# Kernel optimization log

Hardware: AMD Instinct MI355X
Metric: run time of the kernel (lower is better)

The kernel has to match this reference:

```python
import jax, jax.numpy as jnp
import numpy as np

N_EMBD = 768
N_HEAD = 12
B, T = 4, 2048
EPS = 1e-5


def layernorm(x, w, b):
    mu = jnp.mean(x, axis=-1, keepdims=True)
    var = jnp.mean(jnp.square(x - mu), axis=-1, keepdims=True)
    return (x - mu) * jax.lax.rsqrt(var + EPS) * w + b


def setup_inputs() -> dict:
    key = jax.random.key(0)
    ks = jax.random.split(key, 6)
    C = N_EMBD
    s = 0.02
    return {
        "x": jax.random.normal(ks[0], (B, T, C), jnp.float32),
        "ln1_w": jnp.ones((C,), jnp.float32),
        "ln1_b": jnp.zeros((C,), jnp.float32),
        "W_qkv": jax.random.normal(ks[1], (C, 3 * C), jnp.float32) * s,
        "b_qkv": jnp.zeros((3 * C,), jnp.float32),
        "W_attnproj": jax.random.normal(ks[2], (C, C), jnp.float32) * s,
        "b_attnproj": jnp.zeros((C,), jnp.float32),
        "ln2_w": jnp.ones((C,), jnp.float32),
        "ln2_b": jnp.zeros((C,), jnp.float32),
        "W_fc": jax.random.normal(ks[3], (C, 4 * C), jnp.float32) * s,
        "b_fc": jnp.zeros((4 * C,), jnp.float32),
        "W_mlpproj": jax.random.normal(ks[4], (4 * C, C), jnp.float32) * s,
        "b_mlpproj": jnp.zeros((C,), jnp.float32),
    }


def reference(x, ln1_w, ln1_b, W_qkv, b_qkv, W_attnproj, b_attnproj,
              ln2_w, ln2_b, W_fc, b_fc, W_mlpproj, b_mlpproj):
    Bx, Tx, C = x.shape
    H = N_HEAD
    Dh = C // H

    # --- attention branch ---
    h = layernorm(x, ln1_w, ln1_b)
    qkv = h @ W_qkv + b_qkv                       # [B, T, 3C]
    q, k, v = jnp.split(qkv, 3, axis=-1)
    q = q.reshape(Bx, Tx, H, Dh).transpose(0, 2, 1, 3)  # [B, H, T, Dh]
    k = k.reshape(Bx, Tx, H, Dh).transpose(0, 2, 1, 3)
    v = v.reshape(Bx, Tx, H, Dh).transpose(0, 2, 1, 3)
    att = jnp.einsum('bhqd,bhkd->bhqk', q, k) * (1.0 / np.sqrt(Dh))
    att = jax.nn.softmax(att, axis=-1)            # full softmax attention (no mask)
    y = jnp.einsum('bhqk,bhkd->bhqd', att, v)     # [B, H, T, Dh]
    y = y.transpose(0, 2, 1, 3).reshape(Bx, Tx, C)
    y = y @ W_attnproj + b_attnproj
    x = x + y

    # --- MLP branch ---
    h = layernorm(x, ln2_w, ln2_b)
    h = jax.nn.gelu(h @ W_fc + b_fc, approximate=False)
    h = h @ W_mlpproj + b_mlpproj
    return x + h
```

## Files before the change

### kernel.cpp

```cpp
#include <hip/hip_runtime.h>

typedef __bf16 bf16x8 __attribute__((ext_vector_type(8)));
typedef __bf16 bf16x4 __attribute__((ext_vector_type(4)));
typedef float f32x4 __attribute__((ext_vector_type(4)));
typedef unsigned short u16;
typedef unsigned long long u64;

#define GL2LDS(gp, lp) __builtin_amdgcn_global_load_lds(                      \
    (const __attribute__((address_space(1))) void*)(gp),                      \
    (__attribute__((address_space(3))) void*)(lp), 16, 0, 0)

__device__ __forceinline__ u16 f2u(float f) {
    __bf16 h = (__bf16)f;
    return __builtin_bit_cast(u16, h);
}

__device__ __forceinline__ float fexp2(float x) {
    float r;
    asm("v_exp_f32 %0, %1" : "=v"(r) : "v"(x));
    return r;
}

__device__ __forceinline__ float frcp(float x) {
    float r;
    asm("v_rcp_f32 %0, %1" : "=v"(r) : "v"(x));
    return r;
}

__device__ __forceinline__ float gelu(float x) {
    const float a = x * x;
    const float b = fmaf(a, 0.10294323f, 2.30220795f);
    const float u = fexp2(x * b);
    const float r = frcp(1.0f + u);
    return (x > 8.0f) ? x : x * u * r;
}

template <int N>
__device__ __forceinline__ void waitv() {
    if constexpr (N == 0) asm volatile("s_waitcnt vmcnt(0)" ::: "memory");
    else if constexpr (N == 4) asm volatile("s_waitcnt vmcnt(4)" ::: "memory");
    else if constexpr (N == 5) asm volatile("s_waitcnt vmcnt(5)" ::: "memory");
    else if constexpr (N == 6) asm volatile("s_waitcnt vmcnt(6)" ::: "memory");
}

__device__ __forceinline__ f32x4 mfma16(bf16x8 a, bf16x8 b, f32x4 c) {
    return __builtin_amdgcn_mfma_f32_16x16x32_bf16(a, b, c, 0, 0, 0);
}

__global__ __launch_bounds__(256) void transpose_kernel(
    const float* __restrict__ W, u16* __restrict__ Wt, int K, int N) {
    __shared__ float tile[32][33];
    const int tx = threadIdx.x & 31, ty = threadIdx.x >> 5;
    const int n0 = blockIdx.x * 32, k0 = blockIdx.y * 32;
#pragma unroll
    for (int i = 0; i < 4; i++)
        tile[ty + 8 * i][tx] = W[(size_t)(k0 + ty + 8 * i) * N + n0 + tx];
    __syncthreads();
#pragma unroll
    for (int i = 0; i < 4; i++)
        Wt[(size_t)(n0 + ty + 8 * i) * K + k0 + tx] = f2u(tile[tx][ty + 8 * i]);
}

__global__ __launch_bounds__(256) void ln_kernel(
    const float* __restrict__ xin, const float* __restrict__ wgt,
    const float* __restrict__ bia, u16* __restrict__ outp) {
    const int row = blockIdx.x, t = threadIdx.x;
    const float* xr = xin + (size_t)row * 768;
    float v0 = xr[t], v1 = xr[t + 256], v2 = xr[t + 512];
    float s = v0 + v1 + v2;
    float ss = v0 * v0 + v1 * v1 + v2 * v2;
#pragma unroll
    for (int off = 32; off; off >>= 1) {
        s += __shfl_xor(s, off);
        ss += __shfl_xor(ss, off);
    }
    __shared__ float red[8];
    const int w = t >> 6;
    if ((t & 63) == 0) { red[w] = s; red[4 + w] = ss; }
    __syncthreads();
    s  = red[0] + red[1] + red[2] + red[3];
    ss = red[4] + red[5] + red[6] + red[7];
    const float mu = s * (1.f / 768.f);
    const float var = ss * (1.f / 768.f) - mu * mu;
    const float rs = rsqrtf(var + 1e-5f);
    u16* orow = outp + (size_t)row * 768;
    orow[t]       = f2u((v0 - mu) * rs * wgt[t]       + bia[t]);
    orow[t + 256] = f2u((v1 - mu) * rs * wgt[t + 256] + bia[t + 256]);
    orow[t + 512] = f2u((v2 - mu) * rs * wgt[t + 512] + bia[t + 512]);
}

template <int EPI>
__global__ __launch_bounds__(256, 3) void gemm96(
    const u16* __restrict__ A, const u16* __restrict__ Bt,
    const float* __restrict__ bias, void* __restrict__ outp,
    u16* __restrict__ vt, int M, int N, int K) {
    __shared__ __align__(16) u16 As[2][4096];
    __shared__ __align__(16) u16 Bs[2][6144];
    const int t = threadIdx.x;
    const int lane = t & 63, w = t >> 6;
    const int wg0 = blockIdx.y * gridDim.x + blockIdx.x;
    const int xcd = wg0 & 7, loc = wg0 >> 3;
    const int gx = gridDim.x, gy = gridDim.y;
    const int m0 = (xcd * (gy >> 3) + loc / gx) * 128;
    const int n0 = (loc % gx) * 192;
    const int wm = (w >> 1) * 64, wn = (w & 1) * 96;
    const int lq = lane & 15, g = lane >> 4;

    f32x4 acc[4][6];
#pragma unroll
    for (int i = 0; i < 4; i++)
#pragma unroll
        for (int j = 0; j < 6; j++) acc[i][j] = (f32x4){0.f, 0.f, 0.f, 0.f};

    const int srow = t >> 2;
    const int scol = ((t & 3) ^ ((t >> 3) & 3)) * 8;
    const u16* gA0 = A + (size_t)(m0 + srow) * K + scol;
    const u16* gA1 = A + (size_t)(m0 + 64 + srow) * K + scol;
    const u16* gB0 = Bt + (size_t)(n0 + srow) * K + scol;
    const u16* gB1 = Bt + (size_t)(n0 + 64 + srow) * K + scol;
    const u16* gB2 = Bt + (size_t)(n0 + 128 + srow) * K + scol;

    const int cph = (g ^ ((lq >> 1) & 3)) << 4;
    const int KT = K >> 5;

#define STAGE96(buf, kt)                                                      \
    do {                                                                      \
        const int ko_ = (kt) << 5;                                            \
        GL2LDS(gA0 + ko_, (char*)As[buf] + w * 1024);                         \
        GL2LDS(gA1 + ko_, (char*)As[buf] + 4096 + w * 1024);                  \
        GL2LDS(gB0 + ko_, (char*)Bs[buf] + w * 1024);                         \
        GL2LDS(gB1 + ko_, (char*)Bs[buf] + 4096 + w * 1024);                  \
        GL2LDS(gB2 + ko_, (char*)Bs[buf] + 8192 + w * 1024);                  \
    } while (0)

    STAGE96(0, 0);
    STAGE96(1, 1);
    for (int kt = 0; kt < KT; ++kt) {
        if (kt + 1 < KT) waitv<5>(); else waitv<0>();
        __builtin_amdgcn_s_barrier();
        __builtin_amdgcn_sched_barrier(0);
        const char* rA = (char*)As[kt & 1] + (wm + lq) * 64 + cph;
        const char* rB = (char*)Bs[kt & 1] + (wn + lq) * 64 + cph;
        bf16x8 af[4];
#pragma unroll
        for (int m = 0; m < 4; m++) af[m] = *(const bf16x8*)(rA + m * 1024);
        __builtin_amdgcn_s_setprio(1);
#pragma unroll
        for (int n = 0; n < 6; n++) {
            const bf16x8 bfr = *(const bf16x8*)(rB + n * 1024);
#pragma unroll
            for (int m = 0; m < 4; m++)
                acc[m][n] = mfma16(af[m], bfr, acc[m][n]);
        }
        __builtin_amdgcn_s_setprio(0);
        __builtin_amdgcn_sched_barrier(0);
        __builtin_amdgcn_s_barrier();
        if (kt + 2 < KT) STAGE96(kt & 1, kt + 2);
    }
#undef STAGE96

#pragma unroll
    for (int n = 0; n < 6; n++) {
        const int col = n0 + wn + 16 * n + lq;
        const float bv = bias[col];
#pragma unroll
        for (int m = 0; m < 4; m++) {
            const int rbase = m0 + wm + 16 * m + 4 * g;
            if constexpr (EPI == 0) {
                if (col < 1536) {
                    const float qs = (col < 768) ? 0.18033688f : 1.0f;
#pragma unroll
                    for (int r = 0; r < 4; r++) {
                        const size_t idx = (size_t)(rbase + r) * N + col;
                        ((u16*)outp)[idx] = f2u((acc[m][n][r] + bv) * qs);
                    }
                } else {
                    const int d = col - 1536;
                    bf16x4 pk;
#pragma unroll
                    for (int r = 0; r < 4; r++)
                        pk[r] = (__bf16)(acc[m][n][r] + bv);
                    u16* vrow = vt +
                        ((size_t)((rbase >> 11) * 12 + (d >> 6)) * 64 + (d & 63)) * 2048 +
                        (rbase & 2047);
                    *(u64*)vrow = __builtin_bit_cast(u64, pk);
                }
            } else {
#pragma unroll
                for (int r = 0; r < 4; r++) {
                    const size_t idx = (size_t)(rbase + r) * N + col;
                    ((u16*)outp)[idx] = f2u(gelu(acc[m][n][r] + bv));
                }
            }
        }
    }
}

__global__ __launch_bounds__(256, 3) void gemm_k64(
    const u16* __restrict__ A, const u16* __restrict__ Bt,
    const float* __restrict__ bias, const float* __restrict__ res,
    float* __restrict__ outp, int M, int N, int K) {
    __shared__ __align__(16) u16 As[2][4096];
    __shared__ __align__(16) u16 Bs[2][8192];
    const int t = threadIdx.x;
    const int lane = t & 63, w = t >> 6;
    const int wg0 = blockIdx.y * gridDim.x + blockIdx.x;
    const int xcd = wg0 & 7, loc = wg0 >> 3;
    const int gx = gridDim.x, gy = gridDim.y;
    const int m0 = (xcd * (gy >> 3) + loc / gx) * 64;
    const int n0 = (loc % gx) * 128;
    const int wm = (w >> 1) * 32, wn = (w & 1) * 64;
    const int lq = lane & 15, g = lane >> 4;

    f32x4 acc[2][4];
#pragma unroll
    for (int i = 0; i < 2; i++)
#pragma unroll
        for (int j = 0; j < 4; j++) acc[i][j] = (f32x4){0.f, 0.f, 0.f, 0.f};

    const int srow8 = w * 8 + (lane >> 3);
    const int scol = ((lane & 7) ^ (lane >> 3)) * 8;
    const u16* gA_0 = A + (size_t)(m0 + srow8) * K + scol;
    const u16* gA_1 = A + (size_t)(m0 + 32 + srow8) * K + scol;
    const u16* gB_0 = Bt + (size_t)(n0 + srow8) * K + scol;
    const u16* gB_1 = Bt + (size_t)(n0 + 32 + srow8) * K + scol;
    const u16* gB_2 = Bt + (size_t)(n0 + 64 + srow8) * K + scol;
    const u16* gB_3 = Bt + (size_t)(n0 + 96 + srow8) * K + scol;

    const int KT = K >> 6;

#define STAGE64(buf, kt)                                                      \
    do {                                                                      \
        const int ko_ = (kt) << 6;                                            \
        GL2LDS(gA_0 + ko_, (char*)As[buf] + w * 1024);                        \
        GL2LDS(gA_1 + ko_, (char*)As[buf] + 4096 + w * 1024);                 \
        GL2LDS(gB_0 + ko_, (char*)Bs[buf] + w * 1024);                        \
        GL2LDS(gB_1 + ko_, (char*)Bs[buf] + 4096 + w * 1024);                 \
        GL2LDS(gB_2 + ko_, (char*)Bs[buf] + 8192 + w * 1024);                 \
        GL2LDS(gB_3 + ko_, (char*)Bs[buf] + 12288 + w * 1024);                \
    } while (0)

    STAGE64(0, 0);
    STAGE64(1, 1);
    for (int kt = 0; kt < KT; ++kt) {
        if (kt + 1 < KT) waitv<6>(); else waitv<0>();
        __builtin_amdgcn_s_barrier();
        __builtin_amdgcn_sched_barrier(0);
        const char* aB = (char*)As[kt & 1] + (wm + lq) * 128;
        const char* bB = (char*)Bs[kt & 1] + (wn + lq) * 128;
        const int sw = lq & 7;
#pragma unroll
        for (int s = 0; s < 2; s++) {
            const int co = (((s << 2) + g) ^ sw) << 4;
            bf16x8 af[2], bfr[4];
#pragma unroll
            for (int m = 0; m < 2; m++)
                af[m] = *(const bf16x8*)(aB + m * 2048 + co);
#pragma unroll
            for (int n = 0; n < 4; n++)
                bfr[n] = *(const bf16x8*)(bB + n * 2048 + co);
            __builtin_amdgcn_s_setprio(1);
#pragma unroll
            for (int m = 0; m < 2; m++)
#pragma unroll
                for (int n = 0; n < 4; n++)
                    acc[m][n] = mfma16(af[m], bfr[n], acc[m][n]);
            __builtin_amdgcn_s_setprio(0);
        }
        __builtin_amdgcn_sched_barrier(0);
        __builtin_amdgcn_s_barrier();
        if (kt + 2 < KT) STAGE64(kt & 1, kt + 2);
    }
#undef STAGE64

#pragma unroll
    for (int n = 0; n < 4; n++) {
        const int col = n0 + wn + 16 * n + lq;
        const float bv = bias[col];
#pragma unroll
        for (int m = 0; m < 2; m++) {
            const int rbase = m0 + wm + 16 * m + 4 * g;
#pragma unroll
            for (int r = 0; r < 4; r++) {
                const size_t idx = (size_t)(rbase + r) * N + col;
                outp[idx] = acc[m][n][r] + bv + res[idx];
            }
        }
    }
}

__global__ __launch_bounds__(256, 3) void attn_kernel(
    const u16* __restrict__ qkv, const u16* __restrict__ Vt,
    u16* __restrict__ y) {
    __shared__ __align__(16) u16 Ks[8192];
    __shared__ __align__(16) u16 Vts[8192];
    __shared__ __align__(16) u16 Ps[4][2048];
    const int t = threadIdx.x, lane = t & 63, w = t >> 6;
    int wg = blockIdx.y * gridDim.x + blockIdx.x;
    wg = (wg & 7) * ((gridDim.x * gridDim.y) >> 3) + (wg >> 3);
    const int bh = wg / gridDim.x;
    const int b = bh / 12, h = bh % 12;
    const int q0 = (wg % gridDim.x) * 128 + w * 32;
    const int lq = lane & 15, g = lane >> 4;
    const int swz = (lq & 7) << 4;

    bf16x8 qf[2][2];
#pragma unroll
    for (int qh = 0; qh < 2; qh++) {
        const u16* qp =
            qkv + (size_t)(b * 2048 + q0 + qh * 16 + lq) * 2304 + h * 64 + g * 8;
        qf[qh][0] = *(const bf16x8*)(qp);
        qf[qh][1] = *(const bf16x8*)(qp + 32);
    }
    bf16x8 ones;
#pragma unroll
    for (int i = 0; i < 8; i++) ones[i] = (__bf16)1.0f;

    f32x4 acc_o[2][4], acc_s[2];
#pragma unroll
    for (int qh = 0; qh < 2; qh++) {
        acc_s[qh] = (f32x4){0.f, 0.f, 0.f, 0.f};
#pragma unroll
        for (int f = 0; f < 4; f++) acc_o[qh][f] = (f32x4){0.f, 0.f, 0.f, 0.f};
    }

    const int srow = t >> 3, sc = (t & 7) ^ (srow & 7);
    const u16* kg = qkv + 768 + h * 64 + sc * 8 + (size_t)(b * 2048 + srow) * 2304;
    const int vrow = t >> 4, vc = (t & 15) ^ (vrow & 7);
    const u16* vg = Vt + (size_t)(bh * 64 + vrow) * 2048 + vc * 8;

    for (int kt = 0; kt < 16; ++kt) {
        const int k0 = kt * 128;
#pragma unroll
        for (int i = 0; i < 4; i++)
            GL2LDS(kg + (size_t)(k0 + 32 * i) * 2304,
                   (char*)Ks + i * 4096 + w * 1024);
#pragma unroll
        for (int j = 0; j < 4; j++)
            GL2LDS(vg + k0 + j * 32768, (char*)Vts + j * 4096 + w * 1024);
        waitv<0>();
        __builtin_amdgcn_s_barrier();
        __builtin_amdgcn_sched_barrier(0);

#pragma unroll
        for (int half = 0; half < 2; half++) {
            const char* KB = (const char*)Ks + half * 64 * 128;
            f32x4 st[2][4];
            __builtin_amdgcn_s_setprio(1);
#pragma unroll
            for (int kb = 0; kb < 4; kb++) {
                st[0][kb] = (f32x4){0.f, 0.f, 0.f, 0.f};
                st[1][kb] = (f32x4){0.f, 0.f, 0.f, 0.f};
                const char* kr = KB + (kb * 16 + lq) * 128;
#pragma unroll
                for (int dh = 0; dh < 2; dh++) {
                    const bf16x8 kf =
                        *(const bf16x8*)(kr + ((((dh << 2) + g) << 4) ^ swz));
                    st[0][kb] = mfma16(kf, qf[0][dh], st[0][kb]);
                    st[1][kb] = mfma16(kf, qf[1][dh], st[1][kb]);
                }
            }
            __builtin_amdgcn_s_setprio(0);

#pragma unroll
            for (int qh = 0; qh < 2; qh++) {
                char* pw = (char*)Ps[w] + (qh * 16 + lq) * 128 + ((g & 1) << 3);
#pragma unroll
                for (int kb = 0; kb < 4; kb++) {
                    bf16x4 pb;
#pragma unroll
                    for (int r = 0; r < 4; r++)
                        pb[r] = (__bf16)fexp2(st[qh][kb][r]);
                    *(u64*)(pw + ((((kb << 1) + (g >> 1)) << 4) ^ swz)) =
                        __builtin_bit_cast(u64, pb);
                }
            }

            __builtin_amdgcn_s_setprio(1);
#pragma unroll
            for (int kk = 0; kk < 2; kk++) {
                bf16x8 vf[4];
#pragma unroll
                for (int f = 0; f < 4; f++)
                    vf[f] = *(const bf16x8*)(
                        (const char*)Vts + (16 * f + lq) * 256 +
                        ((((half << 3) + (kk << 2) + g) ^ (lq & 7)) << 4));
                const int co = ((kk << 2) + g) << 4;
#pragma unroll
                for (int qh = 0; qh < 2; qh++) {
                    const bf16x8 pf = *(const bf16x8*)(
                        (const char*)Ps[w] + (qh * 16 + lq) * 128 + (co ^ swz));
#pragma unroll
                    for (int f = 0; f < 4; f++)
                        acc_o[qh][f] = mfma16(vf[f], pf, acc_o[qh][f]);
                    acc_s[qh] = mfma16(ones, pf, acc_s[qh]);
                }
            }
            __builtin_amdgcn_s_setprio(0);
        }
        __builtin_amdgcn_sched_barrier(0);
        __builtin_amdgcn_s_barrier();
    }

#pragma unroll
    for (int qh = 0; qh < 2; qh++) {
        const float rinv = frcp(acc_s[qh][0]);
        char* yb = (char*)(y + (size_t)(b * 2048 + q0 + qh * 16 + lq) * 768 +
                           h * 64);
#pragma unroll
        for (int f = 0; f < 4; f++) {
            bf16x4 pk;
#pragma unroll
            for (int r = 0; r < 4; r++) pk[r] = (__bf16)(acc_o[qh][f][r] * rinv);
            *(u64*)(yb + f * 32 + g * 8) = __builtin_bit_cast(u64, pk);
        }
    }
}

extern "C" void kernel_launch(void* const* d_in, const int* in_sizes, int n_in,
                              void* d_out, int out_size, void* d_ws,
                              size_t ws_size, hipStream_t stream) {
    const float* x    = (const float*)d_in[0];
    const float* ln1w = (const float*)d_in[1];
    const float* ln1b = (const float*)d_in[2];
    const float* Wqkv = (const float*)d_in[3];
    const float* bqkv = (const float*)d_in[4];
    const float* Wap  = (const float*)d_in[5];
    const float* bap  = (const float*)d_in[6];
    const float* ln2w = (const float*)d_in[7];
    const float* ln2b = (const float*)d_in[8];
    const float* Wfc  = (const float*)d_in[9];
    const float* bfc  = (const float*)d_in[10];
    const float* Wmp  = (const float*)d_in[11];
    const float* bmp  = (const float*)d_in[12];
    float* out = (float*)d_out;

    char* ws = (char*)d_ws;
    u16* Wt_qkv = (u16*)(ws);
    u16* Wt_ap  = (u16*)(ws + 3538944);
    u16* Wt_fc  = (u16*)(ws + 4718592);
    u16* Wt_mp  = (u16*)(ws + 9437184);
    u16* bufA   = (u16*)(ws + 14155776);
    u16* bufB   = (u16*)(ws + 26738688);
    u16* VtBuf  = (u16*)(ws + 64487424);

    transpose_kernel<<<dim3(72, 24), 256, 0, stream>>>(Wqkv, Wt_qkv, 768, 2304);
    transpose_kernel<<<dim3(24, 24), 256, 0, stream>>>(Wap, Wt_ap, 768, 768);
    transpose_kernel<<<dim3(96, 24), 256, 0, stream>>>(Wfc, Wt_fc, 768, 3072);
    transpose_kernel<<<dim3(24, 96), 256, 0, stream>>>(Wmp, Wt_mp, 3072, 768);

    ln_kernel<<<8192, 256, 0, stream>>>(x, ln1w, ln1b, bufA);
    gemm96<0><<<dim3(12, 64), 256, 0, stream>>>(
        bufA, Wt_qkv, bqkv, bufB, VtBuf, 8192, 2304, 768);
    attn_kernel<<<dim3(16, 48), 256, 0, stream>>>(bufB, VtBuf, bufA);
    gemm_k64<<<dim3(6, 128), 256, 0, stream>>>(
        bufA, Wt_ap, bap, x, out, 8192, 768, 768);
    ln_kernel<<<8192, 256, 0, stream>>>(out, ln2w, ln2b, bufA);
    gemm96<2><<<dim3(16, 64), 256, 0, stream>>>(
        bufA, Wt_fc, bfc, bufB, nullptr, 8192, 3072, 768);
    gemm_k64<<<dim3(6, 128), 256, 0, stream>>>(
        bufB, Wt_mp, bmp, out, out, 8192, 768, 3072);
}
```

Before: 262.7 us.

## Split KV range across warp pairs in attention, each warp covering 64 queries

Each warp now handles 64 query rows instead of 32, and the four warps split the key/value sequence into two halves, so warps 0/1 and 2/3 share query blocks but process different KV ranges. Per iteration, each half's K/V tile is 64 keys instead of one 128-key tile, so every K and V fragment read from LDS feeds twice as many queries. Partial outputs and denominators from warps 2/3 are reduced through shared memory at the end. This costs more accumulator registers (acc_o doubles), which may hurt occupancy at launch bounds (256,3), and adds an LDS reduction step.

```diff
diff --git a/kernel.cpp b/kernel.cpp
--- a/kernel.cpp
+++ b/kernel.cpp
@@ -292,21 +292,22 @@
 __global__ __launch_bounds__(256, 3) void attn_kernel(
     const u16* __restrict__ qkv, const u16* __restrict__ Vt,
     u16* __restrict__ y) {
-    __shared__ __align__(16) u16 Ks[8192];
-    __shared__ __align__(16) u16 Vts[8192];
+    __shared__ __align__(16) u16 Ks[2][4096];
+    __shared__ __align__(16) u16 Vts[2][4096];
     __shared__ __align__(16) u16 Ps[4][2048];
     const int t = threadIdx.x, lane = t & 63, w = t >> 6;
     int wg = blockIdx.y * gridDim.x + blockIdx.x;
     wg = (wg & 7) * ((gridDim.x * gridDim.y) >> 3) + (wg >> 3);
     const int bh = wg / gridDim.x;
     const int b = bh / 12, h = bh % 12;
-    const int q0 = (wg % gridDim.x) * 128 + w * 32;
+    const int q0 = (wg % gridDim.x) * 128 + (w & 1) * 64;
+    const int khalf = w >> 1;
     const int lq = lane & 15, g = lane >> 4;
     const int swz = (lq & 7) << 4;
 
-    bf16x8 qf[2][2];
-#pragma unroll
-    for (int qh = 0; qh < 2; qh++) {
+    bf16x8 qf[4][2];
+#pragma unroll
+    for (int qh = 0; qh < 4; qh++) {
         const u16* qp =
             qkv + (size_t)(b * 2048 + q0 + qh * 16 + lq) * 2304 + h * 64 + g * 8;
         qf[qh][0] = *(const bf16x8*)(qp);
@@ -316,9 +317,9 @@
 #pragma unroll
     for (int i = 0; i < 8; i++) ones[i] = (__bf16)1.0f;
 
-    f32x4 acc_o[2][4], acc_s[2];
-#pragma unroll
-    for (int qh = 0; qh < 2; qh++) {
+    f32x4 acc_o[4][4], acc_s[4];
+#pragma unroll
+    for (int qh = 0; qh < 4; qh++) {
         acc_s[qh] = (f32x4){0.f, 0.f, 0.f, 0.f};
 #pragma unroll
         for (int f = 0; f < 4; f++) acc_o[qh][f] = (f32x4){0.f, 0.f, 0.f, 0.f};
@@ -326,25 +327,29 @@
 
     const int srow = t >> 3, sc = (t & 7) ^ (srow & 7);
     const u16* kg = qkv + 768 + h * 64 + sc * 8 + (size_t)(b * 2048 + srow) * 2304;
-    const int vrow = t >> 4, vc = (t & 15) ^ (vrow & 7);
-    const u16* vg = Vt + (size_t)(bh * 64 + vrow) * 2048 + vc * 8;
+    const u16* vg = Vt + (size_t)(bh * 64 + srow) * 2048 + sc * 8;
+
+    const char* KB = (const char*)Ks + khalf * 8192;
+    const char* VB = (const char*)Vts + khalf * 8192;
 
     for (int kt = 0; kt < 16; ++kt) {
-        const int k0 = kt * 128;
-#pragma unroll
-        for (int i = 0; i < 4; i++)
-            GL2LDS(kg + (size_t)(k0 + 32 * i) * 2304,
-                   (char*)Ks + i * 4096 + w * 1024);
-#pragma unroll
-        for (int j = 0; j < 4; j++)
-            GL2LDS(vg + k0 + j * 32768, (char*)Vts + j * 4096 + w * 1024);
+#pragma unroll
+        for (int hh = 0; hh < 2; hh++) {
+            const int kb0 = hh * 1024 + kt * 64;
+            GL2LDS(kg + (size_t)kb0 * 2304,
+                   (char*)Ks + hh * 8192 + w * 1024);
+            GL2LDS(kg + (size_t)(kb0 + 32) * 2304,
+                   (char*)Ks + hh * 8192 + 4096 + w * 1024);
+            GL2LDS(vg + kb0, (char*)Vts + hh * 8192 + w * 1024);
+            GL2LDS(vg + kb0 + 32 * 2048,
+                   (char*)Vts + hh * 8192 + 4096 + w * 1024);
+        }
         waitv<0>();
         __builtin_amdgcn_s_barrier();
         __builtin_amdgcn_sched_barrier(0);
 
 #pragma unroll
-        for (int half = 0; half < 2; half++) {
-            const char* KB = (const char*)Ks + half * 64 * 128;
+        for (int p = 0; p < 2; p++) {
             f32x4 st[2][4];
             __builtin_amdgcn_s_setprio(1);
 #pragma unroll
@@ -356,21 +361,21 @@
                 for (int dh = 0; dh < 2; dh++) {
                     const bf16x8 kf =
                         *(const bf16x8*)(kr + ((((dh << 2) + g) << 4) ^ swz));
-                    st[0][kb] = mfma16(kf, qf[0][dh], st[0][kb]);
-                    st[1][kb] = mfma16(kf, qf[1][dh], st[1][kb]);
+                    st[0][kb] = mfma16(kf, qf[2 * p][dh], st[0][kb]);
+                    st[1][kb] = mfma16(kf, qf[2 * p + 1][dh], st[1][kb]);
                 }
             }
             __builtin_amdgcn_s_setprio(0);
 
 #pragma unroll
-            for (int qh = 0; qh < 2; qh++) {
-                char* pw = (char*)Ps[w] + (qh * 16 + lq) * 128 + ((g & 1) << 3);
+            for (int e = 0; e < 2; e++) {
+                char* pw = (char*)Ps[w] + (e * 16 + lq) * 128 + ((g & 1) << 3);
 #pragma unroll
                 for (int kb = 0; kb < 4; kb++) {
                     bf16x4 pb;
 #pragma unroll
                     for (int r = 0; r < 4; r++)
-                        pb[r] = (__bf16)fexp2(st[qh][kb][r]);
+                        pb[r] = (__bf16)fexp2(st[e][kb][r]);
                     *(u64*)(pw + ((((kb << 1) + (g >> 1)) << 4) ^ swz)) =
                         __builtin_bit_cast(u64, pb);
                 }
@@ -379,21 +384,21 @@
             __builtin_amdgcn_s_setprio(1);
 #pragma unroll
             for (int kk = 0; kk < 2; kk++) {
+                const int co = ((kk << 2) + g) << 4;
                 bf16x8 vf[4];
 #pragma unroll
                 for (int f = 0; f < 4; f++)
-                    vf[f] = *(const bf16x8*)(
-                        (const char*)Vts + (16 * f + lq) * 256 +
-                        ((((half << 3) + (kk << 2) + g) ^ (lq & 7)) << 4));
-                const int co = ((kk << 2) + g) << 4;
-#pragma unroll
-                for (int qh = 0; qh < 2; qh++) {
+                    vf[f] = *(const bf16x8*)(VB + (16 * f + lq) * 128 +
+                                             (co ^ swz));
+#pragma unroll
+                for (int e = 0; e < 2; e++) {
                     const bf16x8 pf = *(const bf16x8*)(
-                        (const char*)Ps[w] + (qh * 16 + lq) * 128 + (co ^ swz));
+                        (const char*)Ps[w] + (e * 16 + lq) * 128 + (co ^ swz));
 #pragma unroll
                     for (int f = 0; f < 4; f++)
-                        acc_o[qh][f] = mfma16(vf[f], pf, acc_o[qh][f]);
-                    acc_s[qh] = mfma16(ones, pf, acc_s[qh]);
+                        acc_o[2 * p + e][f] =
+                            mfma16(vf[f], pf, acc_o[2 * p + e][f]);
+                    acc_s[2 * p + e] = mfma16(ones, pf, acc_s[2 * p + e]);
                 }
             }
             __builtin_amdgcn_s_setprio(0);
@@ -402,17 +407,38 @@
         __builtin_amdgcn_s_barrier();
     }
 
-#pragma unroll
-    for (int qh = 0; qh < 2; qh++) {
-        const float rinv = frcp(acc_s[qh][0]);
-        char* yb = (char*)(y + (size_t)(b * 2048 + q0 + qh * 16 + lq) * 768 +
-                           h * 64);
-#pragma unroll
-        for (int f = 0; f < 4; f++) {
-            bf16x4 pk;
-#pragma unroll
-            for (int r = 0; r < 4; r++) pk[r] = (__bf16)(acc_o[qh][f][r] * rinv);
-            *(u64*)(yb + f * 32 + g * 8) = __builtin_bit_cast(u64, pk);
+    if (w >= 2) {
+        char* base = (w == 2) ? (char*)Ks : (char*)Vts;
+#pragma unroll
+        for (int qh = 0; qh < 4; qh++)
+#pragma unroll
+            for (int f = 0; f < 4; f++)
+                *(f32x4*)(base + (((qh << 2) + f) * 64 + lane) * 16) =
+                    acc_o[qh][f];
+        float* db = (float*)Ps[0] + (w - 2) * 256;
+#pragma unroll
+        for (int qh = 0; qh < 4; qh++) db[qh * 64 + lane] = acc_s[qh][0];
+    }
+    __syncthreads();
+    if (w < 2) {
+        const char* base = (w == 0) ? (const char*)Ks : (const char*)Vts;
+        const float* db = (const float*)Ps[0] + w * 256;
+#pragma unroll
+        for (int qh = 0; qh < 4; qh++) {
+            const float den = acc_s[qh][0] + db[qh * 64 + lane];
+            const float rinv = frcp(den);
+            char* yb = (char*)(y + (size_t)(b * 2048 + q0 + qh * 16 + lq) * 768 +
+                               h * 64);
+#pragma unroll
+            for (int f = 0; f < 4; f++) {
+                const f32x4 other =
+                    *(const f32x4*)(base + (((qh << 2) + f) * 64 + lane) * 16);
+                bf16x4 pk;
+#pragma unroll
+                for (int r = 0; r < 4; r++)
+                    pk[r] = (__bf16)((acc_o[qh][f][r] + other[r]) * rinv);
+                *(u64*)(yb + f * 32 + g * 8) = __builtin_bit_cast(u64, pk);
+            }
         }
     }
 }
```

Measured after the change: 278.8 us. 6.1% more time.
